# Performance work log

Measured on AMD Instinct MI355X. Metric: run time of the kernel, lower is better.

## Reference

```python
import jax, jax.numpy as jnp
import numpy as np
import math

B, N = 64, 16384
POS_IN, HID, DIR_IN = 63, 128, 27
COLOR_IN = HID + DIR_IN  # 155
POS_W, POS_B = POS_IN * HID, HID          # 8064, 128
SIG_W, SIG_B = HID * 1, 1                  # 128, 1
COL_W, COL_B = COLOR_IN * 3, 3             # 465... actually 155*3=465? no: 465
TOTAL = POS_W + POS_B + SIG_W + SIG_B + COL_W + COL_B  # 8717


def pos_encode(x, num_freqs):
    # x: [..., 3] -> [..., 3 + 2*3*num_freqs], order: x, (sin f0, cos f0, sin f1, cos f1, ...)
    freqs = (2.0 ** jnp.arange(num_freqs, dtype=x.dtype)) * math.pi  # [L]
    xb = x[..., None, :] * freqs[:, None]                            # [..., L, 3]
    sc = jnp.stack([jnp.sin(xb), jnp.cos(xb)], axis=-2)              # [..., L, 2, 3]
    sc = sc.reshape(*x.shape[:-1], num_freqs * 2 * x.shape[-1])
    return jnp.concatenate([x, sc], axis=-1)


def setup_inputs() -> dict:
    key = jax.random.key(0)
    k1, k2, k3 = jax.random.split(key, 3)
    positions = jax.random.normal(k1, (B, N, 3), dtype=jnp.float32)
    directions = jax.random.normal(k2, (B, N, 3), dtype=jnp.float32)
    params = jax.random.normal(k3, (B, TOTAL), dtype=jnp.float32) * 0.1
    return {"positions": positions, "directions": directions, "params": params}


def reference(positions, directions, params):
    pos_enc = pos_encode(positions, 10)   # [B, N, 63]
    dir_enc = pos_encode(directions, 4)   # [B, N, 27]

    i = 0
    pw = params[:, i:i + POS_W].reshape(B, HID, POS_IN); i += POS_W
    pb = params[:, i:i + POS_B]; i += POS_B
    sw = params[:, i:i + SIG_W].reshape(B, 1, HID); i += SIG_W
    sb = params[:, i:i + SIG_B]; i += SIG_B
    cw = params[:, i:i + COL_W].reshape(B, 3, COLOR_IN); i += COL_W
    cb = params[:, i:i + COL_B]

    h = jnp.einsum('bnd,bhd->bnh', pos_enc, pw) + pb[:, None, :]
    h = jax.nn.relu(h)                                   # [B, N, 128]
    sigma = jnp.einsum('bnh,boh->bno', h, sw) + sb[:, None, :]  # [B, N, 1]
    h_dir = jnp.concatenate([h, dir_enc], axis=-1)       # [B, N, 155]
    rgb = jnp.einsum('bnc,boc->bno', h_dir, cw) + cb[:, None, :]
    rgb = jax.nn.sigmoid(rgb)                            # [B, N, 3]
    return sigma, rgb
```

## Files before the change

kernel.cpp:

```cpp
#include <hip/hip_runtime.h>
#include <hip/hip_bf16.h>


#define NB 64
#define NRAY 16384
#define NTOTAL 8789

typedef short bf16x8 __attribute__((ext_vector_type(8)));
typedef float f32x16 __attribute__((ext_vector_type(16)));

union U8 { unsigned u[4]; bf16x8 v; };

__device__ __forceinline__ unsigned pk2(float a, float b) {
    float2 t; t.x = a; t.y = b;
    __hip_bfloat162 h = __float22bfloat162_rn(t);
    return *reinterpret_cast<unsigned*>(&h);
}

#define MFMA __builtin_amdgcn_mfma_f32_32x32x16_bf16

__global__ __launch_bounds__(256, 2) void nerf_mfma_kernel(
    const float* __restrict__ pos,
    const float* __restrict__ dir,
    const float* __restrict__ params,
    float* __restrict__ out)
{
    const int tid  = threadIdx.x;
    const int lane = tid & 63;
    const int wid  = tid >> 6;
    const int hi   = lane >> 5;
    const int l31  = lane & 31;

    const int b     = blockIdx.x >> 4;
    const int chunk = (blockIdx.x & 15) << 10;
    const float* __restrict__ p = params + b * NTOTAL;

    __shared__ uint4 encs[2048];
    __shared__ unsigned hawLds[256];
    char* encb = reinterpret_cast<char*>(encs);
    const char* hawb = reinterpret_cast<const char*>(hawLds);

    if (tid < 64) {
        const int s  = tid & 7;
        const int hh = (tid >> 3) & 1;
        const int r  = tid >> 4;
        const float* w2 = (r == 0) ? (p + 8192) : (p + 8321 + (r - 1) * 155);
        const int base = 32 * (s >> 1) + 16 * (s & 1) + 4 * hh;
        unsigned* dst = &hawLds[(((s << 1) + hh) * 4 + r) * 4];
        #pragma unroll
        for (int j = 0; j < 4; ++j) {
            const int i0 = 2 * j, i1 = 2 * j + 1;
            dst[j] = pk2(w2[base + (i0 & 3) + 8 * (i0 >> 2)],
                         w2[base + (i1 & 3) + 8 * (i1 >> 2)]);
        }
    }

    bf16x8 aw[4][4];
    #pragma unroll
    for (int mt = 0; mt < 4; ++mt) {
        const int hrow = mt * 32 + l31;
        const float* wrow = p + hrow * 63;
        const float bias = p[8064 + hrow];
        #pragma unroll
        for (int ks = 0; ks < 4; ++ks) {
            U8 u;
            #pragma unroll
            for (int j = 0; j < 4; ++j) {
                const int k0 = ks * 16 + hi * 8 + 2 * j;
                const int k1 = k0 + 1;
                const float e0 = (k0 < 3) ? wrow[k0] : (k0 == 3 ? bias : wrow[k0 - 1]);
                const float e1 = (k1 < 3) ? wrow[k1] : (k1 == 3 ? bias : wrow[k1 - 1]);
                u.u[j] = pk2(e0, e1);
            }
            aw[mt][ks] = u.v;
        }
    }

    f32x16 FZ;
    #pragma unroll
    for (int i = 0; i < 16; ++i) FZ[i] = 0.f;

    const float sb  = p[8320];
    const float cb0 = p[8786], cb1 = p[8787], cb2 = p[8788];
    const float* __restrict__ cwr  = p + 8321 + 128;
    const float* __restrict__ cwg  = p + 8321 + 155 + 128;
    const float* __restrict__ cwb2 = p + 8321 + 310 + 128;

    const int rayBlock = b * NRAY + chunk;
    float* __restrict__ rgbout = out + (long)NB * NRAY;
    const long pb0 = (long)(rayBlock + tid) * 3;
    const int hoff = hi * 64 + (l31 & 3) * 16;

    auto encode_row = [&](const float3 Pv) {
        const int swz = (tid & 7) << 4;
        char* myrow = encb + tid * 128;
        float s0 = __builtin_amdgcn_sinf(0.5f * Pv.x), c0 = __builtin_amdgcn_cosf(0.5f * Pv.x);
        float s1 = __builtin_amdgcn_sinf(0.5f * Pv.y), c1 = __builtin_amdgcn_cosf(0.5f * Pv.y);
        float s2 = __builtin_amdgcn_sinf(0.5f * Pv.z), c2 = __builtin_amdgcn_cosf(0.5f * Pv.z);
        unsigned wb[4];
        wb[0] = pk2(Pv.x, Pv.y);
        wb[1] = pk2(Pv.z, 1.0f);
        #pragma unroll
        for (int f = 0; f < 10; ++f) {
            const int w = 2 + 3 * f;
            wb[(w + 0) & 3] = pk2(s0, s1);
            if (((w + 0) & 3) == 3) {
                uint4 v; v.x = wb[0]; v.y = wb[1]; v.z = wb[2]; v.w = wb[3];
                *reinterpret_cast<uint4*>(myrow + ((((w + 0) >> 2) * 16) ^ swz)) = v;
            }
            wb[(w + 1) & 3] = pk2(s2, c0);
            if (((w + 1) & 3) == 3) {
                uint4 v; v.x = wb[0]; v.y = wb[1]; v.z = wb[2]; v.w = wb[3];
                *reinterpret_cast<uint4*>(myrow + ((((w + 1) >> 2) * 16) ^ swz)) = v;
            }
            wb[(w + 2) & 3] = pk2(c1, c2);
            if (((w + 2) & 3) == 3) {
                uint4 v; v.x = wb[0]; v.y = wb[1]; v.z = wb[2]; v.w = wb[3];
                *reinterpret_cast<uint4*>(myrow + ((((w + 2) >> 2) * 16) ^ swz)) = v;
            }
            if (f < 9) {
                float t;
                t = 2.f * s0 * c0; c0 = fmaf(-2.f * s0, s0, 1.f); s0 = t;
                t = 2.f * s1 * c1; c1 = fmaf(-2.f * s1, s1, 1.f); s1 = t;
                t = 2.f * s2 * c2; c2 = fmaf(-2.f * s2, s2, 1.f); s2 = t;
            }
        }
    };

    float3 Pc = *reinterpret_cast<const float3*>(pos + pb0);
    float3 Pn = *reinterpret_cast<const float3*>(pos + pb0 + 768);
    float3 Dc = *reinterpret_cast<const float3*>(dir + pb0);
    float3 Dn = *reinterpret_cast<const float3*>(dir + pb0 + 768);
    encode_row(Pc);
    __syncthreads();

    #pragma unroll 1
    for (int it = 0; it < 4; ++it) {
        const int ray = rayBlock + it * 256 + tid;

        float3 Pn2, Dn2;
        if (it < 2) {
            Pn2 = *reinterpret_cast<const float3*>(pos + pb0 + (it + 2) * 768);
            Dn2 = *reinterpret_cast<const float3*>(dir + pb0 + (it + 2) * 768);
        }

        bf16x8 be0[4], be1[4];
        {
            const int row0 = wid * 64 + l31;
            const int swz0 = (row0 & 7) << 4;
            const int row1 = row0 + 32;
            const int swz1 = (row1 & 7) << 4;
            #pragma unroll
            for (int ks = 0; ks < 4; ++ks) {
                be0[ks] = *reinterpret_cast<const bf16x8*>(
                    encb + row0 * 128 + ((ks * 32 + hi * 16) ^ swz0));
                be1[ks] = *reinterpret_cast<const bf16x8*>(
                    encb + row1 * 128 + ((ks * 32 + hi * 16) ^ swz1));
            }
        }

        if (it < 3) encode_row(Pn);

        float crd = 0.f, cgd = 0.f, cbd = 0.f;
        {
            float s0 = __builtin_amdgcn_sinf(0.5f * Dc.x), c0 = __builtin_amdgcn_cosf(0.5f * Dc.x);
            float s1 = __builtin_amdgcn_sinf(0.5f * Dc.y), c1 = __builtin_amdgcn_cosf(0.5f * Dc.y);
            float s2 = __builtin_amdgcn_sinf(0.5f * Dc.z), c2 = __builtin_amdgcn_cosf(0.5f * Dc.z);
            crd = fmaf(Dc.x, cwr[0], crd);  cgd = fmaf(Dc.x, cwg[0], cgd);  cbd = fmaf(Dc.x, cwb2[0], cbd);
            crd = fmaf(Dc.y, cwr[1], crd);  cgd = fmaf(Dc.y, cwg[1], cgd);  cbd = fmaf(Dc.y, cwb2[1], cbd);
            crd = fmaf(Dc.z, cwr[2], crd);  cgd = fmaf(Dc.z, cwg[2], cgd);  cbd = fmaf(Dc.z, cwb2[2], cbd);
            #pragma unroll
            for (int f = 0; f < 4; ++f) {
                const int j = 3 + 6 * f;
                crd = fmaf(s0, cwr[j+0], crd); cgd = fmaf(s0, cwg[j+0], cgd); cbd = fmaf(s0, cwb2[j+0], cbd);
                crd = fmaf(s1, cwr[j+1], crd); cgd = fmaf(s1, cwg[j+1], cgd); cbd = fmaf(s1, cwb2[j+1], cbd);
                crd = fmaf(s2, cwr[j+2], crd); cgd = fmaf(s2, cwg[j+2], cgd); cbd = fmaf(s2, cwb2[j+2], cbd);
                crd = fmaf(c0, cwr[j+3], crd); cgd = fmaf(c0, cwg[j+3], cgd); cbd = fmaf(c0, cwb2[j+3], cbd);
                crd = fmaf(c1, cwr[j+4], crd); cgd = fmaf(c1, cwg[j+4], cgd); cbd = fmaf(c1, cwb2[j+4], cbd);
                crd = fmaf(c2, cwr[j+5], crd); cgd = fmaf(c2, cwg[j+5], cgd); cbd = fmaf(c2, cwb2[j+5], cbd);
                if (f < 3) {
                    float t;
                    t = 2.f * s0 * c0; c0 = fmaf(-2.f * s0, s0, 1.f); s0 = t;
                    t = 2.f * s1 * c1; c1 = fmaf(-2.f * s1, s1, 1.f); s1 = t;
                    t = 2.f * s2 * c2; c2 = fmaf(-2.f * s2, s2, 1.f); s2 = t;
                }
            }
        }

        __builtin_amdgcn_s_setprio(1);
        f32x16 hacc0, hacc1;
        #pragma unroll
        for (int mt = 0; mt < 4; ++mt) {
            f32x16 a0 = MFMA(aw[mt][0], be0[0], FZ, 0, 0, 0);
            f32x16 a1 = MFMA(aw[mt][0], be1[0], FZ, 0, 0, 0);
            a0 = MFMA(aw[mt][1], be0[1], a0, 0, 0, 0);
            a1 = MFMA(aw[mt][1], be1[1], a1, 0, 0, 0);
            a0 = MFMA(aw[mt][2], be0[2], a0, 0, 0, 0);
            a1 = MFMA(aw[mt][2], be1[2], a1, 0, 0, 0);
            a0 = MFMA(aw[mt][3], be0[3], a0, 0, 0, 0);
            a1 = MFMA(aw[mt][3], be1[3], a1, 0, 0, 0);

            #pragma unroll
            for (int t = 0; t < 2; ++t) {
                const int rb = t * 8;
                const int s = 2 * mt + t;
                U8 u0, u1;
                #pragma unroll
                for (int j = 0; j < 4; ++j) {
                    u0.u[j] = pk2(fmaxf(a0[rb + 2 * j], 0.f),
                                  fmaxf(a0[rb + 2 * j + 1], 0.f));
                    u1.u[j] = pk2(fmaxf(a1[rb + 2 * j], 0.f),
                                  fmaxf(a1[rb + 2 * j + 1], 0.f));
                }
                const bf16x8 hw = *reinterpret_cast<const bf16x8*>(
                    hawb + s * 128 + hoff);
                hacc0 = MFMA(hw, u0.v, (s == 0) ? FZ : hacc0, 0, 0, 0);
                hacc1 = MFMA(hw, u1.v, (s == 0) ? FZ : hacc1, 0, 0, 0);
            }
        }
        __builtin_amdgcn_s_setprio(0);

        const float hv0 = hi ? hacc1[0] : hacc0[0];
        const float hv1 = hi ? hacc1[1] : hacc0[1];
        const float hv2 = hi ? hacc1[2] : hacc0[2];
        const float hv3 = hi ? hacc1[3] : hacc0[3];

        const float sig = hv0 + sb;
        float cr  = hv1 + cb0 + crd;
        float cg  = hv2 + cb1 + cgd;
        float cbl = hv3 + cb2 + cbd;

        cr  = 1.0f / (1.0f + __expf(-cr));
        cg  = 1.0f / (1.0f + __expf(-cg));
        cbl = 1.0f / (1.0f + __expf(-cbl));

        out[ray] = sig;
        float3 rgbv; rgbv.x = cr; rgbv.y = cg; rgbv.z = cbl;
        *reinterpret_cast<float3*>(rgbout + (long)ray * 3) = rgbv;

        Pn = Pn2; Dc = Dn; Dn = Dn2;
    }
}

extern "C" void kernel_launch(void* const* d_in, const int* in_sizes, int n_in,
                              void* d_out, int out_size, void* d_ws, size_t ws_size,
                              hipStream_t stream) {
    const float* pos    = (const float*)d_in[0];
    const float* dirs   = (const float*)d_in[1];
    const float* params = (const float*)d_in[2];
    float* out = (float*)d_out;

    dim3 grid(1024);
    dim3 block(256);
    nerf_mfma_kernel<<<grid, block, 0, stream>>>(pos, dirs, params, out);
}
```

Baseline: 50.29 us.

## Stage first-layer weights in LDS to cut registers and raise occupancy

The bf16 first-layer weight fragments move from 64 per-thread registers into a swizzled LDS table, which is reloaded per m-tile inside a non-unrolled loop. Launch bounds rise from 2 to 3 blocks per SIMD. The next-tile position/direction prefetch is moved later in the loop and the initial loads are reordered. This trades added LDS traffic and loop overhead in the MFMA section for lower register pressure and more resident waves to hide latency.

```diff
diff --git a/kernel.cpp b/kernel.cpp
--- a/kernel.cpp
+++ b/kernel.cpp
@@ -5,6 +5,7 @@
 #define NB 64
 #define NRAY 16384
 #define NTOTAL 8789
+#define NIT 4
 
 typedef short bf16x8 __attribute__((ext_vector_type(8)));
 typedef float f32x16 __attribute__((ext_vector_type(16)));
@@ -19,7 +20,7 @@
 
 #define MFMA __builtin_amdgcn_mfma_f32_32x32x16_bf16
 
-__global__ __launch_bounds__(256, 2) void nerf_mfma_kernel(
+__global__ __launch_bounds__(256, 3) void nerf_mfma_kernel(
     const float* __restrict__ pos,
     const float* __restrict__ dir,
     const float* __restrict__ params,
@@ -36,8 +37,10 @@
     const float* __restrict__ p = params + b * NTOTAL;
 
     __shared__ uint4 encs[2048];
+    __shared__ uint4 awT[1024];
     __shared__ unsigned hawLds[256];
     char* encb = reinterpret_cast<char*>(encs);
+    const char* awb  = reinterpret_cast<const char*>(awT);
     const char* hawb = reinterpret_cast<const char*>(hawLds);
 
     if (tid < 64) {
@@ -55,24 +58,26 @@
         }
     }
 
-    bf16x8 aw[4][4];
-    #pragma unroll
-    for (int mt = 0; mt < 4; ++mt) {
-        const int hrow = mt * 32 + l31;
-        const float* wrow = p + hrow * 63;
-        const float bias = p[8064 + hrow];
+    {
+        const int h    = tid >> 1;
+        const int half = tid & 1;
+        const float* wrow = p + h * 63;
+        const float bias  = p[8064 + h];
+        char* dst = reinterpret_cast<char*>(awT) + h * 128;
+        const int swz = (h & 7) << 4;
         #pragma unroll
-        for (int ks = 0; ks < 4; ++ks) {
+        for (int c4 = 0; c4 < 4; ++c4) {
+            const int c = half * 4 + c4;
             U8 u;
             #pragma unroll
             for (int j = 0; j < 4; ++j) {
-                const int k0 = ks * 16 + hi * 8 + 2 * j;
-                const int k1 = k0 + 1;
+                const int k0 = 8 * c + 2 * j, k1 = k0 + 1;
                 const float e0 = (k0 < 3) ? wrow[k0] : (k0 == 3 ? bias : wrow[k0 - 1]);
                 const float e1 = (k1 < 3) ? wrow[k1] : (k1 == 3 ? bias : wrow[k1 - 1]);
                 u.u[j] = pk2(e0, e1);
             }
-            aw[mt][ks] = u.v;
+            *reinterpret_cast<uint4*>(dst + ((c * 16) ^ swz)) =
+                *reinterpret_cast<uint4*>(&u);
         }
     }
 
@@ -128,21 +133,15 @@
     };
 
     float3 Pc = *reinterpret_cast<const float3*>(pos + pb0);
+    float3 Dc = *reinterpret_cast<const float3*>(dir + pb0);
+    encode_row(Pc);
     float3 Pn = *reinterpret_cast<const float3*>(pos + pb0 + 768);
-    float3 Dc = *reinterpret_cast<const float3*>(dir + pb0);
     float3 Dn = *reinterpret_cast<const float3*>(dir + pb0 + 768);
-    encode_row(Pc);
     __syncthreads();
 
     #pragma unroll 1
-    for (int it = 0; it < 4; ++it) {
+    for (int it = 0; it < NIT; ++it) {
         const int ray = rayBlock + it * 256 + tid;
-
-        float3 Pn2, Dn2;
-        if (it < 2) {
-            Pn2 = *reinterpret_cast<const float3*>(pos + pb0 + (it + 2) * 768);
-            Dn2 = *reinterpret_cast<const float3*>(dir + pb0 + (it + 2) * 768);
-        }
 
         bf16x8 be0[4], be1[4];
         {
@@ -159,7 +158,7 @@
             }
         }
 
-        if (it < 3) encode_row(Pn);
+        if (it < NIT - 1) encode_row(Pn);
 
         float crd = 0.f, cgd = 0.f, cbd = 0.f;
         {
@@ -187,23 +186,36 @@
             }
         }
 
+        float3 Pn2, Dn2;
+        if (it < NIT - 2) {
+            Pn2 = *reinterpret_cast<const float3*>(pos + pb0 + (it + 2) * 768);
+            Dn2 = *reinterpret_cast<const float3*>(dir + pb0 + (it + 2) * 768);
+        }
+
         __builtin_amdgcn_s_setprio(1);
-        f32x16 hacc0, hacc1;
-        #pragma unroll
+        f32x16 hacc0 = FZ, hacc1 = FZ;
+        #pragma unroll 1
         for (int mt = 0; mt < 4; ++mt) {
-            f32x16 a0 = MFMA(aw[mt][0], be0[0], FZ, 0, 0, 0);
-            f32x16 a1 = MFMA(aw[mt][0], be1[0], FZ, 0, 0, 0);
-            a0 = MFMA(aw[mt][1], be0[1], a0, 0, 0, 0);
-            a1 = MFMA(aw[mt][1], be1[1], a1, 0, 0, 0);
-            a0 = MFMA(aw[mt][2], be0[2], a0, 0, 0, 0);
-            a1 = MFMA(aw[mt][2], be1[2], a1, 0, 0, 0);
-            a0 = MFMA(aw[mt][3], be0[3], a0, 0, 0, 0);
-            a1 = MFMA(aw[mt][3], be1[3], a1, 0, 0, 0);
+            const int arow = (mt << 5) + l31;
+            const int aswz = (arow & 7) << 4;
+            const char* abase = awb + arow * 128;
+            const bf16x8 awf0 = *reinterpret_cast<const bf16x8*>(abase + ((0  + hi * 16) ^ aswz));
+            const bf16x8 awf1 = *reinterpret_cast<const bf16x8*>(abase + ((32 + hi * 16) ^ aswz));
+            const bf16x8 awf2 = *reinterpret_cast<const bf16x8*>(abase + ((64 + hi * 16) ^ aswz));
+            const bf16x8 awf3 = *reinterpret_cast<const bf16x8*>(abase + ((96 + hi * 16) ^ aswz));
+
+            f32x16 a0 = MFMA(awf0, be0[0], FZ, 0, 0, 0);
+            f32x16 a1 = MFMA(awf0, be1[0], FZ, 0, 0, 0);
+            a0 = MFMA(awf1, be0[1], a0, 0, 0, 0);
+            a1 = MFMA(awf1, be1[1], a1, 0, 0, 0);
+            a0 = MFMA(awf2, be0[2], a0, 0, 0, 0);
+            a1 = MFMA(awf2, be1[2], a1, 0, 0, 0);
+            a0 = MFMA(awf3, be0[3], a0, 0, 0, 0);
+            a1 = MFMA(awf3, be1[3], a1, 0, 0, 0);
 
             #pragma unroll
             for (int t = 0; t < 2; ++t) {
                 const int rb = t * 8;
-                const int s = 2 * mt + t;
                 U8 u0, u1;
                 #pragma unroll
                 for (int j = 0; j < 4; ++j) {
@@ -213,9 +225,9 @@
                                   fmaxf(a1[rb + 2 * j + 1], 0.f));
                 }
                 const bf16x8 hw = *reinterpret_cast<const bf16x8*>(
-                    hawb + s * 128 + hoff);
-                hacc0 = MFMA(hw, u0.v, (s == 0) ? FZ : hacc0, 0, 0, 0);
-                hacc1 = MFMA(hw, u1.v, (s == 0) ? FZ : hacc1, 0, 0, 0);
+                    hawb + (2 * mt + t) * 128 + hoff);
+                hacc0 = MFMA(hw, u0.v, hacc0, 0, 0, 0);
+                hacc1 = MFMA(hw, u1.v, hacc1, 0, 0, 0);
             }
         }
         __builtin_amdgcn_s_setprio(0);
```

Result: faster. 45.94 us (-8.6%).
